# Performance work log

Measured on AMD Instinct MI355X. Metric: run time of the kernel, lower is better.

## Reference

```python
import jax, jax.numpy as jnp
import numpy as np

N_SRC = 50000
N_DST = 50000
N_EDGES = 1_600_000
D_IN = 128
D_OUT = 128
NUM_HEADS = 8
SCALE = float((D_OUT // NUM_HEADS) ** 0.5)


def setup_inputs() -> dict:
    key = jax.random.key(0)
    ks = jax.random.split(key, 10)
    s = 1.0 / np.sqrt(D_IN)
    return {
        "src_feat": jax.random.normal(ks[0], (N_SRC, D_IN), dtype=jnp.float32),
        "dst_feat": jax.random.normal(ks[1], (N_DST, D_OUT), dtype=jnp.float32),
        "src_idx": jax.random.randint(ks[2], (N_EDGES,), 0, N_SRC, dtype=jnp.int64),
        "dst_idx": jax.random.randint(ks[3], (N_EDGES,), 0, N_DST, dtype=jnp.int64),
        "Wq": jax.random.normal(ks[4], (D_OUT, D_OUT), dtype=jnp.float32) * s,
        "bq": jnp.zeros((D_OUT,), dtype=jnp.float32),
        "Wk": jax.random.normal(ks[5], (D_OUT, D_IN), dtype=jnp.float32) * s,
        "bk": jnp.zeros((D_OUT,), dtype=jnp.float32),
        "Wv": jax.random.normal(ks[6], (D_OUT, D_IN), dtype=jnp.float32) * s,
        "bv": jnp.zeros((D_OUT,), dtype=jnp.float32),
    }


def reference(src_feat, dst_feat, src_idx, dst_idx, Wq, bq, Wk, bk, Wv, bv):
    # Node-level projections (torch Linear: x @ W.T + b)
    Q = dst_feat @ Wq.T + bq            # [N_dst, D_OUT]
    K = src_feat @ Wk.T + bk            # [N_src, D_OUT]
    V = src_feat @ Wv.T + bv            # [N_src, D_OUT]

    # Edge-wise full-dim dot-product score (heads only affect the scale)
    score = jnp.sum(Q[dst_idx] * K[src_idx], axis=-1) / SCALE  # [E]

    # Segment softmax over incoming edges of each destination node
    m = jax.ops.segment_max(score, dst_idx, num_segments=N_DST)   # [N_dst]
    e = jnp.exp(score - m[dst_idx])                               # [E]
    denom = jax.ops.segment_sum(e, dst_idx, num_segments=N_DST)   # [N_dst]
    attn = e / denom[dst_idx]                                     # [E]

    # Weighted V scatter-sum to destination nodes
    out = jax.ops.segment_sum(attn[:, None] * V[src_idx], dst_idx,
                              num_segments=N_DST)                 # [N_dst, D_OUT]
    return out
```

## Files before the change

### kernel.cpp

```cpp
#include <hip/hip_runtime.h>
#include <hip/hip_bf16.h>


#define D 128
#define E1 4096
#define BCAP 10240
#define LOG2E 1.44269504088896340736f

typedef __attribute__((ext_vector_type(8))) short bf16x8;
typedef __attribute__((ext_vector_type(4))) float f32x4;
typedef __attribute__((ext_vector_type(4))) int v4i;
typedef __attribute__((ext_vector_type(4))) unsigned v4u;

static __device__ __forceinline__ unsigned short f2bf(float f) {
  unsigned u = __float_as_uint(f);
  u += 0x7fff + ((u >> 16) & 1);
  return (unsigned short)(u >> 16);
}
static __device__ __forceinline__ float bfl(unsigned u) {
  return __uint_as_float(u << 16);
}
static __device__ __forceinline__ float bfh(unsigned u) {
  return __uint_as_float(u & 0xffff0000u);
}

template <int CTRL>
static __device__ __forceinline__ float dpp_add(float x) {
  int y = __builtin_amdgcn_update_dpp(0, __float_as_int(x), CTRL, 0xF, 0xF, false);
  return x + __int_as_float(y);
}

static __device__ __forceinline__ float dot8(const float4& qa, const float4& qb,
                                             const v4u k0, const v4u k1) {
  return (qa.x * bfl(k0.x) + qa.y * bfh(k0.x) + qa.z * bfl(k0.y) +
          qa.w * bfh(k0.y)) +
         (qb.x * bfl(k1.x) + qb.y * bfh(k1.x) + qb.z * bfl(k1.y) +
          qb.w * bfh(k1.y));
}

static __device__ __forceinline__ void stage_w(const float* __restrict__ W,
                                               char* lds) {
  const int tid = threadIdx.x;
#pragma unroll
  for (int i = 0; i < 8; ++i) {
    const int g = i * 256 + tid;
    const int r = g >> 4, c16 = g & 15;
    const float4 w0 = *(const float4*)(W + r * 128 + c16 * 8);
    const float4 w1 = *(const float4*)(W + r * 128 + c16 * 8 + 4);
    bf16x8 b;
    b[0] = f2bf(w0.x); b[1] = f2bf(w0.y); b[2] = f2bf(w0.z); b[3] = f2bf(w0.w);
    b[4] = f2bf(w1.x); b[5] = f2bf(w1.y); b[6] = f2bf(w1.z); b[7] = f2bf(w1.w);
    *(bf16x8*)(lds + r * 256 + (((c16 ^ (r & 7)) << 4))) = b;
  }
}

static __device__ __forceinline__ bf16x8 ldw_lds(const char* lds, int n,
                                                 int colbyte) {
  return *(const bf16x8*)(lds + n * 256 + (colbyte ^ ((n & 7) << 4)));
}

static __device__ void bin1_body(
    int bx, int* h, int* basebuf, int* cur, const int* __restrict__ src_idx,
    const int* __restrict__ dst_idx, int* __restrict__ bins,
    int* __restrict__ bcount, int n) {
  const int tid = threadIdx.x;
  const int e0 = bx * E1;
  int dv[16], sv[16];
#pragma unroll
  for (int i = 0; i < 4; ++i) {
    int e = e0 + i * 1024 + tid * 4;
    if (e + 3 < n) {
      v4i d4 = __builtin_nontemporal_load((const v4i*)(dst_idx + e));
      v4i s4 = __builtin_nontemporal_load((const v4i*)(src_idx + e));
      dv[4 * i + 0] = d4.x; dv[4 * i + 1] = d4.y;
      dv[4 * i + 2] = d4.z; dv[4 * i + 3] = d4.w;
      sv[4 * i + 0] = s4.x; sv[4 * i + 1] = s4.y;
      sv[4 * i + 2] = s4.z; sv[4 * i + 3] = s4.w;
    } else {
      for (int k = 0; k < 4; ++k) {
        int ee = e + k;
        dv[4 * i + k] = (ee < n) ? dst_idx[ee] : -1;
        sv[4 * i + k] = (ee < n) ? src_idx[ee] : 0;
      }
    }
  }
  h[tid] = 0;
  __syncthreads();
#pragma unroll
  for (int i = 0; i < 16; ++i)
    if (dv[i] >= 0) atomicAdd(&h[dv[i] >> 8], 1);
  __syncthreads();
  const int c = h[tid];
  if (c > 0) basebuf[tid] = tid * BCAP + atomicAdd(&bcount[tid], c);
  cur[tid] = 0;
  __syncthreads();
#pragma unroll
  for (int i = 0; i < 16; ++i) {
    if (dv[i] >= 0) {
      const int b = dv[i] >> 8;
      const int r = atomicAdd(&cur[b], 1);
      const int off = basebuf[b] + r;
      if (off < (b + 1) * BCAP)
        bins[off] = sv[i] | ((dv[i] & 255) << 17);
    }
  }
}

static __device__ void bin2_body_1k(
    int b, int* smem, const int* __restrict__ bins,
    const int* __restrict__ bcount, int* __restrict__ csr,
    int* __restrict__ rowptr, int n_dst, int n_edges) {
  int* h = smem;
  int* ofs = smem + 256;
  int* cur = smem + 512;
  int* red = smem + 768;
  const int tid = threadIdx.x;

  if (tid < 256) red[tid] = (tid < b) ? min(bcount[tid], BCAP) : 0;
  __syncthreads();
  for (int off = 128; off > 0; off >>= 1) {
    if (tid < off) red[tid] += red[tid + off];
    __syncthreads();
  }
  const int gbase = red[0];
  const int cnt = min(bcount[b], BCAP);
  if (tid < 256) h[tid] = 0;
  __syncthreads();

  const int* bb = bins + b * BCAP;
  for (int i = tid; i < cnt; i += 1024) atomicAdd(&h[(bb[i] >> 17) & 255], 1);
  __syncthreads();

  const int myh = (tid < 256) ? h[tid] : 0;
  if (tid < 256) red[tid] = myh;
  __syncthreads();
  for (int off = 1; off < 256; off <<= 1) {
    int t = (tid >= off && tid < 256) ? red[tid - off] : 0;
    __syncthreads();
    if (tid < 256) red[tid] += t;
    __syncthreads();
  }
  if (tid < 256) {
    ofs[tid] = red[tid] - myh;
    cur[tid] = 0;
    const int d = b * 256 + tid;
    if (d < n_dst) rowptr[d] = gbase + ofs[tid];
    if (b == 0 && tid == 0) rowptr[n_dst] = n_edges;
  }
  __syncthreads();

  for (int i = tid; i < cnt; i += 1024) {
    const int p = bb[i];
    const int j = (p >> 17) & 255;
    const int r = atomicAdd(&cur[j], 1);
    csr[gbase + ofs[j] + r] = p & 0x1ffff;
  }
}

static __device__ void gemm_q_body(
    int bx, char* wlds, const float* __restrict__ X,
    const float* __restrict__ Wf, const float* __restrict__ bias,
    float* __restrict__ out, int N) {
  stage_w(Wf, wlds);
  __syncthreads();

  const int lane = threadIdx.x & 63;
  const int l15 = lane & 15, quad = lane >> 4;
  const int row0 = bx * 64 + (threadIdx.x >> 6) * 16;

  f32x4 acc[8];
#pragma unroll
  for (int t = 0; t < 8; ++t) acc[t] = (f32x4){0.f, 0.f, 0.f, 0.f};

  int ar = row0 + l15;
  if (ar >= N) ar = N - 1;
  const float* ap = X + (size_t)ar * D + quad * 8;

#pragma unroll
  for (int kc = 0; kc < 4; ++kc) {
    float4 a0 = *(const float4*)(ap + kc * 32);
    float4 a1 = *(const float4*)(ap + kc * 32 + 4);
    bf16x8 a;
    a[0] = f2bf(a0.x); a[1] = f2bf(a0.y); a[2] = f2bf(a0.z); a[3] = f2bf(a0.w);
    a[4] = f2bf(a1.x); a[5] = f2bf(a1.y); a[6] = f2bf(a1.z); a[7] = f2bf(a1.w);
    const int cb = kc * 64 + quad * 16;
#pragma unroll
    for (int t = 0; t < 8; ++t) {
      bf16x8 b = ldw_lds(wlds, t * 16 + l15, cb);
      acc[t] = __builtin_amdgcn_mfma_f32_16x16x32_bf16(a, b, acc[t], 0, 0, 0);
    }
  }
#pragma unroll
  for (int t = 0; t < 8; ++t) {
    const int c = t * 16 + l15;
    const float bc = bias[c];
#pragma unroll
    for (int r = 0; r < 4; ++r) {
      const int row = row0 + quad * 4 + r;
      if (row < N) out[(size_t)row * D + c] = acc[t][r] + bc;
    }
  }
}

static __device__ void gemm_kv_body(
    int bx, char* wlds, const float* __restrict__ X,
    const float* __restrict__ Wkf, const float* __restrict__ bk,
    const float* __restrict__ Wvf, const float* __restrict__ bv,
    unsigned short* __restrict__ KV, int N) {
  char* wk = wlds;
  char* wv = wlds + 32768;
  stage_w(Wkf, wk);
  stage_w(Wvf, wv);
  __syncthreads();

  const int tid = threadIdx.x;
  const int lane = tid & 63;
  const int l15 = lane & 15, quad = lane >> 4;
  const int wave = tid >> 6;
  const int row0 = bx * 64 + wave * 16;

  f32x4 accK[8], accV[8];
#pragma unroll
  for (int t = 0; t < 8; ++t) {
    accK[t] = (f32x4){0.f, 0.f, 0.f, 0.f};
    accV[t] = (f32x4){0.f, 0.f, 0.f, 0.f};
  }

  int ar = row0 + l15;
  if (ar >= N) ar = N - 1;
  const float* ap = X + (size_t)ar * D + quad * 8;

#pragma unroll
  for (int kc = 0; kc < 4; ++kc) {
    float4 a0 = *(const float4*)(ap + kc * 32);
    float4 a1 = *(const float4*)(ap + kc * 32 + 4);
    bf16x8 a;
    a[0] = f2bf(a0.x); a[1] = f2bf(a0.y); a[2] = f2bf(a0.z); a[3] = f2bf(a0.w);
    a[4] = f2bf(a1.x); a[5] = f2bf(a1.y); a[6] = f2bf(a1.z); a[7] = f2bf(a1.w);
    const int cb = kc * 64 + quad * 16;
#pragma unroll
    for (int t = 0; t < 8; ++t) {
      const int n = t * 16 + l15;
      bf16x8 b0 = ldw_lds(wk, n, cb);
      bf16x8 b1 = ldw_lds(wv, n, cb);
      accK[t] = __builtin_amdgcn_mfma_f32_16x16x32_bf16(a, b0, accK[t], 0, 0, 0);
      accV[t] = __builtin_amdgcn_mfma_f32_16x16x32_bf16(a, b1, accV[t], 0, 0, 0);
    }
  }

  __syncthreads();
  unsigned short (*stage)[256] = (unsigned short(*)[256])wlds;
#pragma unroll
  for (int t = 0; t < 8; ++t) {
    const int c = t * 16 + l15;
    const float bkc = bk[c], bvc = bv[c];
    const int ki = ((c >> 2) << 3) + (c & 3);
#pragma unroll
    for (int r = 0; r < 4; ++r) {
      const int lr = wave * 16 + quad * 4 + r;
      stage[lr][ki] = f2bf(accK[t][r] + bkc);
      stage[lr][ki + 4] = f2bf(accV[t][r] + bvc);
    }
  }
  __syncthreads();
  const int row_base = bx * 64;
#pragma unroll
  for (int i = 0; i < 8; ++i) {
    int idx = i * 256 + tid;
    int lr = idx >> 5;
    int c8 = (idx & 31) << 3;
    int grow = row_base + lr;
    if (grow < N)
      *(f32x4*)(KV + (size_t)grow * 256 + c8) = *(const f32x4*)&stage[lr][c8];
  }
}

static __device__ void fused_body(
    int v, const float* __restrict__ Q, const unsigned short* __restrict__ KV,
    const int* __restrict__ csr, const int* __restrict__ rowptr,
    float* __restrict__ out, int n_dst) {
  const int lane = threadIdx.x & 63;
  const int g = lane >> 4;
  const int gl = lane & 15;
  int d = v * 4 + (threadIdx.x >> 6);
  if (d >= n_dst) return;
  d = __builtin_amdgcn_readfirstlane(d);
  const int start = __builtin_amdgcn_readfirstlane(rowptr[d]);
  const int n = __builtin_amdgcn_readfirstlane(rowptr[d + 1]) - start;

  const float qs = 0.25f * LOG2E;
  float4 q0 = *(const float4*)(Q + (size_t)d * D + 4 * gl);
  float4 q1 = *(const float4*)(Q + (size_t)d * D + 64 + 4 * gl);
  q0.x *= qs; q0.y *= qs; q0.z *= qs; q0.w *= qs;
  q1.x *= qs; q1.y *= qs; q1.z *= qs; q1.w *= qs;

  f32x4 acc0 = (f32x4){0.f, 0.f, 0.f, 0.f};
  f32x4 acc1 = (f32x4){0.f, 0.f, 0.f, 0.f};
  float den = 0.f;
  const int* cp = csr + start;

  for (int base = 0; base < n; base += 64) {
    const int il = base + lane;
    const int iv = __builtin_nontemporal_load(cp + ((il < n) ? il : (n - 1)));
    const int m = min(64, n - base);
    for (int j = 0; j < m; j += 16) {
      const int s0 = __shfl(iv, j + g, 64);
      const int s1 = __shfl(iv, j + 4 + g, 64);
      const int s2 = __shfl(iv, j + 8 + g, 64);
      const int s3 = __shfl(iv, j + 12 + g, 64);
      const unsigned short* r0 = KV + (size_t)s0 * 256 + gl * 8;
      const unsigned short* r1 = KV + (size_t)s1 * 256 + gl * 8;
      const unsigned short* r2 = KV + (size_t)s2 * 256 + gl * 8;
      const unsigned short* r3 = KV + (size_t)s3 * 256 + gl * 8;
      const v4u a0 = *(const v4u*)(r0);
      const v4u a1 = *(const v4u*)(r0 + 128);
      const v4u b0 = *(const v4u*)(r1);
      const v4u b1 = *(const v4u*)(r1 + 128);
      const v4u c0 = *(const v4u*)(r2);
      const v4u c1 = *(const v4u*)(r2 + 128);
      const v4u e0 = *(const v4u*)(r3);
      const v4u e1 = *(const v4u*)(r3 + 128);

      float p0 = dot8(q0, q1, a0, a1);
      float p1 = dot8(q0, q1, b0, b1);
      float p2 = dot8(q0, q1, c0, c1);
      float p3 = dot8(q0, q1, e0, e1);

      p0 = dpp_add<0xB1>(p0);  p1 = dpp_add<0xB1>(p1);
      p2 = dpp_add<0xB1>(p2);  p3 = dpp_add<0xB1>(p3);
      p0 = dpp_add<0x4E>(p0);  p1 = dpp_add<0x4E>(p1);
      p2 = dpp_add<0x4E>(p2);  p3 = dpp_add<0x4E>(p3);
      p0 = dpp_add<0x141>(p0); p1 = dpp_add<0x141>(p1);
      p2 = dpp_add<0x141>(p2); p3 = dpp_add<0x141>(p3);
      p0 = dpp_add<0x140>(p0); p1 = dpp_add<0x140>(p1);
      p2 = dpp_add<0x140>(p2); p3 = dpp_add<0x140>(p3);

      const float w0 = (j + g < m)      ? exp2f(p0) : 0.f;
      const float w1 = (j + 4 + g < m)  ? exp2f(p1) : 0.f;
      const float w2 = (j + 8 + g < m)  ? exp2f(p2) : 0.f;
      const float w3 = (j + 12 + g < m) ? exp2f(p3) : 0.f;

      acc0[0] += w0 * bfl(a0.z) + w1 * bfl(b0.z) + w2 * bfl(c0.z) + w3 * bfl(e0.z);
      acc0[1] += w0 * bfh(a0.z) + w1 * bfh(b0.z) + w2 * bfh(c0.z) + w3 * bfh(e0.z);
      acc0[2] += w0 * bfl(a0.w) + w1 * bfl(b0.w) + w2 * bfl(c0.w) + w3 * bfl(e0.w);
      acc0[3] += w0 * bfh(a0.w) + w1 * bfh(b0.w) + w2 * bfh(c0.w) + w3 * bfh(e0.w);
      acc1[0] += w0 * bfl(a1.z) + w1 * bfl(b1.z) + w2 * bfl(c1.z) + w3 * bfl(e1.z);
      acc1[1] += w0 * bfh(a1.z) + w1 * bfh(b1.z) + w2 * bfh(c1.z) + w3 * bfh(e1.z);
      acc1[2] += w0 * bfl(a1.w) + w1 * bfl(b1.w) + w2 * bfl(c1.w) + w3 * bfl(e1.w);
      acc1[3] += w0 * bfh(a1.w) + w1 * bfh(b1.w) + w2 * bfh(c1.w) + w3 * bfh(e1.w);
      den += (w0 + w1) + (w2 + w3);
    }
  }

#pragma unroll
  for (int msk = 16; msk <= 32; msk <<= 1) {
    acc0[0] += __shfl_xor(acc0[0], msk, 64);
    acc0[1] += __shfl_xor(acc0[1], msk, 64);
    acc0[2] += __shfl_xor(acc0[2], msk, 64);
    acc0[3] += __shfl_xor(acc0[3], msk, 64);
    acc1[0] += __shfl_xor(acc1[0], msk, 64);
    acc1[1] += __shfl_xor(acc1[1], msk, 64);
    acc1[2] += __shfl_xor(acc1[2], msk, 64);
    acc1[3] += __shfl_xor(acc1[3], msk, 64);
    den += __shfl_xor(den, msk, 64);
  }

  if (lane < 16) {
    const float r = (n > 0) ? 1.0f / den : 0.f;
    f32x4 o0 = (f32x4){acc0[0] * r, acc0[1] * r, acc0[2] * r, acc0[3] * r};
    f32x4 o1 = (f32x4){acc1[0] * r, acc1[1] * r, acc1[2] * r, acc1[3] * r};
    __builtin_nontemporal_store(o0, (f32x4*)(out + (size_t)d * D + 4 * gl));
    __builtin_nontemporal_store(o1,
                                (f32x4*)(out + (size_t)d * D + 64 + 4 * gl));
  }
}


__global__ __launch_bounds__(256) void front_kernel(
    const int* __restrict__ src_idx, const int* __restrict__ dst_idx,
    int* __restrict__ bins, int* __restrict__ bcount, int n_edges,
    const float* __restrict__ dst_feat, const float* __restrict__ Wq,
    const float* __restrict__ bq, float* __restrict__ Q, int n_dst,
    const float* __restrict__ src_feat, const float* __restrict__ Wk,
    const float* __restrict__ bk, const float* __restrict__ Wv,
    const float* __restrict__ bv, unsigned short* __restrict__ KV, int n_src,
    int g1, int gq) {
  __shared__ char wlds[65536];
  const int b = blockIdx.x;
  if (b < g1) {
    int* sh = (int*)wlds;
    bin1_body(b, sh, sh + 256, sh + 512, src_idx, dst_idx, bins, bcount,
              n_edges);
  } else if (b < g1 + gq) {
    gemm_q_body(b - g1, wlds, dst_feat, Wq, bq, Q, n_dst);
  } else {
    gemm_kv_body(b - g1 - gq, wlds, src_feat, Wk, bk, Wv, bv, KV, n_src);
  }
}

__global__ __launch_bounds__(1024) void bin2_kernel(
    const int* __restrict__ bins, const int* __restrict__ bcount,
    int* __restrict__ csr, int* __restrict__ rowptr, int n_dst, int n_edges) {
  __shared__ int sh[1024];
  bin2_body_1k(blockIdx.x, sh, bins, bcount, csr, rowptr, n_dst, n_edges);
}

__global__ __launch_bounds__(256) void fused_agg_kernel(
    const float* __restrict__ Q, const unsigned short* __restrict__ KV,
    const int* __restrict__ csr, const int* __restrict__ rowptr,
    float* __restrict__ out, int n_dst) {
  fused_body(blockIdx.x, Q, KV, csr, rowptr, out, n_dst);
}

extern "C" void kernel_launch(void* const* d_in, const int* in_sizes, int n_in,
                              void* d_out, int out_size, void* d_ws,
                              size_t ws_size, hipStream_t stream) {
  const float* src_feat = (const float*)d_in[0];
  const float* dst_feat = (const float*)d_in[1];
  const int* src_idx = (const int*)d_in[2];
  const int* dst_idx = (const int*)d_in[3];
  const float* Wq = (const float*)d_in[4];
  const float* bq = (const float*)d_in[5];
  const float* Wk = (const float*)d_in[6];
  const float* bk = (const float*)d_in[7];
  const float* Wv = (const float*)d_in[8];
  const float* bv = (const float*)d_in[9];

  const int n_src = in_sizes[0] / D;
  const int n_dst = in_sizes[1] / D;
  const int n_edges = in_sizes[2];
  const int nbk = (n_dst + 255) >> 8;

  float* out = (float*)d_out;

  float* Q = (float*)d_ws;
  unsigned short* KV = (unsigned short*)(Q + (size_t)n_dst * D);
  int* bcount = (int*)(KV + (size_t)n_src * 256);
  int* rowptr = bcount + 256;
  int* csr = rowptr + (n_dst + 1);
  int* bins = csr + n_edges;

  (void)hipMemsetAsync(bcount, 0, 256 * sizeof(int), stream);

  dim3 blk(256);
  const int g1 = (n_edges + E1 - 1) / E1;
  const int gq = (n_dst + 63) / 64;
  const int gkv = (n_src + 63) / 64;
  const int nf = (n_dst + 3) / 4;

  front_kernel<<<dim3(g1 + gq + gkv), blk, 0, stream>>>(
      src_idx, dst_idx, bins, bcount, n_edges, dst_feat, Wq, bq, Q, n_dst,
      src_feat, Wk, bk, Wv, bv, KV, n_src, g1, gq);

  bin2_kernel<<<dim3(nbk), dim3(1024), 0, stream>>>(bins, bcount, csr, rowptr,
                                                    n_dst, n_edges);

  fused_agg_kernel<<<dim3(nf), blk, 0, stream>>>(Q, KV, csr, rowptr, out,
                                                 n_dst);
}
```

Before: 267.0 us.

## Split bin2 buckets into quarters and amortize weight staging over 256-row GEMM blocks

The second binning pass now launches four 512-thread blocks per bucket. Each block rebuilds the bucket histogram but writes only the CSR entries and rowptr values for its own quarter of destinations, which spreads the work over more CUs. The Q and KV projection blocks each process 256 rows in four 64-row chunks, so the weight matrices are staged into LDS once per 256 rows instead of once per 64. KV output staging moves to a separate LDS region and is written out in half-tiles, raising front-kernel LDS to 80KB, which may reduce occupancy for the binning blocks that share that kernel.

```diff
diff --git a/kernel.cpp b/kernel.cpp
--- a/kernel.cpp
+++ b/kernel.cpp
@@ -106,29 +106,31 @@
   }
 }
 
-static __device__ void bin2_body_1k(
+static __device__ void bin2_body_q(
     int b, int* smem, const int* __restrict__ bins,
     const int* __restrict__ bcount, int* __restrict__ csr,
     int* __restrict__ rowptr, int n_dst, int n_edges) {
+  const int bucket = b >> 2;
+  const int quarter = b & 3;
   int* h = smem;
   int* ofs = smem + 256;
   int* cur = smem + 512;
   int* red = smem + 768;
   const int tid = threadIdx.x;
 
-  if (tid < 256) red[tid] = (tid < b) ? min(bcount[tid], BCAP) : 0;
+  if (tid < 256) red[tid] = (tid < bucket) ? min(bcount[tid], BCAP) : 0;
   __syncthreads();
   for (int off = 128; off > 0; off >>= 1) {
     if (tid < off) red[tid] += red[tid + off];
     __syncthreads();
   }
   const int gbase = red[0];
-  const int cnt = min(bcount[b], BCAP);
+  const int cnt = min(bcount[bucket], BCAP);
   if (tid < 256) h[tid] = 0;
   __syncthreads();
 
-  const int* bb = bins + b * BCAP;
-  for (int i = tid; i < cnt; i += 1024) atomicAdd(&h[(bb[i] >> 17) & 255], 1);
+  const int* bb = bins + bucket * BCAP;
+  for (int i = tid; i < cnt; i += 512) atomicAdd(&h[(bb[i] >> 17) & 255], 1);
   __syncthreads();
 
   const int myh = (tid < 256) ? h[tid] : 0;
@@ -143,17 +145,19 @@
   if (tid < 256) {
     ofs[tid] = red[tid] - myh;
     cur[tid] = 0;
-    const int d = b * 256 + tid;
-    if (d < n_dst) rowptr[d] = gbase + ofs[tid];
-    if (b == 0 && tid == 0) rowptr[n_dst] = n_edges;
-  }
-  __syncthreads();
-
-  for (int i = tid; i < cnt; i += 1024) {
+    const int d = bucket * 256 + tid;
+    if ((tid >> 6) == quarter && d < n_dst) rowptr[d] = gbase + ofs[tid];
+  }
+  if (b == 0 && tid == 0) rowptr[n_dst] = n_edges;
+  __syncthreads();
+
+  for (int i = tid; i < cnt; i += 512) {
     const int p = bb[i];
     const int j = (p >> 17) & 255;
-    const int r = atomicAdd(&cur[j], 1);
-    csr[gbase + ofs[j] + r] = p & 0x1ffff;
+    if ((j >> 6) == quarter) {
+      const int r = atomicAdd(&cur[j], 1);
+      csr[gbase + ofs[j] + r] = p & 0x1ffff;
+    }
   }
 }
 
@@ -166,38 +170,42 @@
 
   const int lane = threadIdx.x & 63;
   const int l15 = lane & 15, quad = lane >> 4;
-  const int row0 = bx * 64 + (threadIdx.x >> 6) * 16;
-
-  f32x4 acc[8];
-#pragma unroll
-  for (int t = 0; t < 8; ++t) acc[t] = (f32x4){0.f, 0.f, 0.f, 0.f};
-
-  int ar = row0 + l15;
-  if (ar >= N) ar = N - 1;
-  const float* ap = X + (size_t)ar * D + quad * 8;
-
-#pragma unroll
-  for (int kc = 0; kc < 4; ++kc) {
-    float4 a0 = *(const float4*)(ap + kc * 32);
-    float4 a1 = *(const float4*)(ap + kc * 32 + 4);
-    bf16x8 a;
-    a[0] = f2bf(a0.x); a[1] = f2bf(a0.y); a[2] = f2bf(a0.z); a[3] = f2bf(a0.w);
-    a[4] = f2bf(a1.x); a[5] = f2bf(a1.y); a[6] = f2bf(a1.z); a[7] = f2bf(a1.w);
-    const int cb = kc * 64 + quad * 16;
+  const int wave = threadIdx.x >> 6;
+
+#pragma unroll
+  for (int ch = 0; ch < 4; ++ch) {
+    const int row0 = bx * 256 + ch * 64 + wave * 16;
+    f32x4 acc[8];
+#pragma unroll
+    for (int t = 0; t < 8; ++t) acc[t] = (f32x4){0.f, 0.f, 0.f, 0.f};
+
+    int ar = row0 + l15;
+    if (ar >= N) ar = N - 1;
+    const float* ap = X + (size_t)ar * D + quad * 8;
+
+#pragma unroll
+    for (int kc = 0; kc < 4; ++kc) {
+      float4 a0 = *(const float4*)(ap + kc * 32);
+      float4 a1 = *(const float4*)(ap + kc * 32 + 4);
+      bf16x8 a;
+      a[0] = f2bf(a0.x); a[1] = f2bf(a0.y); a[2] = f2bf(a0.z); a[3] = f2bf(a0.w);
+      a[4] = f2bf(a1.x); a[5] = f2bf(a1.y); a[6] = f2bf(a1.z); a[7] = f2bf(a1.w);
+      const int cb = kc * 64 + quad * 16;
+#pragma unroll
+      for (int t = 0; t < 8; ++t) {
+        bf16x8 b = ldw_lds(wlds, t * 16 + l15, cb);
+        acc[t] = __builtin_amdgcn_mfma_f32_16x16x32_bf16(a, b, acc[t], 0, 0, 0);
+      }
+    }
 #pragma unroll
     for (int t = 0; t < 8; ++t) {
-      bf16x8 b = ldw_lds(wlds, t * 16 + l15, cb);
-      acc[t] = __builtin_amdgcn_mfma_f32_16x16x32_bf16(a, b, acc[t], 0, 0, 0);
-    }
-  }
-#pragma unroll
-  for (int t = 0; t < 8; ++t) {
-    const int c = t * 16 + l15;
-    const float bc = bias[c];
-#pragma unroll
-    for (int r = 0; r < 4; ++r) {
-      const int row = row0 + quad * 4 + r;
-      if (row < N) out[(size_t)row * D + c] = acc[t][r] + bc;
+      const int c = t * 16 + l15;
+      const float bc = bias[c];
+#pragma unroll
+      for (int r = 0; r < 4; ++r) {
+        const int row = row0 + quad * 4 + r;
+        if (row < N) out[(size_t)row * D + c] = acc[t][r] + bc;
+      }
     }
   }
 }
@@ -209,6 +217,7 @@
     unsigned short* __restrict__ KV, int N) {
   char* wk = wlds;
   char* wv = wlds + 32768;
+  unsigned short (*stage)[256] = (unsigned short(*)[256])(wlds + 65536);
   stage_w(Wkf, wk);
   stage_w(Wvf, wv);
   __syncthreads();
@@ -217,61 +226,71 @@
   const int lane = tid & 63;
   const int l15 = lane & 15, quad = lane >> 4;
   const int wave = tid >> 6;
-  const int row0 = bx * 64 + wave * 16;
-
-  f32x4 accK[8], accV[8];
-#pragma unroll
-  for (int t = 0; t < 8; ++t) {
-    accK[t] = (f32x4){0.f, 0.f, 0.f, 0.f};
-    accV[t] = (f32x4){0.f, 0.f, 0.f, 0.f};
-  }
-
-  int ar = row0 + l15;
-  if (ar >= N) ar = N - 1;
-  const float* ap = X + (size_t)ar * D + quad * 8;
-
-#pragma unroll
-  for (int kc = 0; kc < 4; ++kc) {
-    float4 a0 = *(const float4*)(ap + kc * 32);
-    float4 a1 = *(const float4*)(ap + kc * 32 + 4);
-    bf16x8 a;
-    a[0] = f2bf(a0.x); a[1] = f2bf(a0.y); a[2] = f2bf(a0.z); a[3] = f2bf(a0.w);
-    a[4] = f2bf(a1.x); a[5] = f2bf(a1.y); a[6] = f2bf(a1.z); a[7] = f2bf(a1.w);
-    const int cb = kc * 64 + quad * 16;
+
+#pragma unroll
+  for (int ch = 0; ch < 4; ++ch) {
+    const int row0 = bx * 256 + ch * 64 + wave * 16;
+    f32x4 accK[8], accV[8];
 #pragma unroll
     for (int t = 0; t < 8; ++t) {
-      const int n = t * 16 + l15;
-      bf16x8 b0 = ldw_lds(wk, n, cb);
-      bf16x8 b1 = ldw_lds(wv, n, cb);
-      accK[t] = __builtin_amdgcn_mfma_f32_16x16x32_bf16(a, b0, accK[t], 0, 0, 0);
-      accV[t] = __builtin_amdgcn_mfma_f32_16x16x32_bf16(a, b1, accV[t], 0, 0, 0);
-    }
-  }
-
-  __syncthreads();
-  unsigned short (*stage)[256] = (unsigned short(*)[256])wlds;
-#pragma unroll
-  for (int t = 0; t < 8; ++t) {
-    const int c = t * 16 + l15;
-    const float bkc = bk[c], bvc = bv[c];
-    const int ki = ((c >> 2) << 3) + (c & 3);
-#pragma unroll
-    for (int r = 0; r < 4; ++r) {
-      const int lr = wave * 16 + quad * 4 + r;
-      stage[lr][ki] = f2bf(accK[t][r] + bkc);
-      stage[lr][ki + 4] = f2bf(accV[t][r] + bvc);
-    }
-  }
-  __syncthreads();
-  const int row_base = bx * 64;
-#pragma unroll
-  for (int i = 0; i < 8; ++i) {
-    int idx = i * 256 + tid;
-    int lr = idx >> 5;
-    int c8 = (idx & 31) << 3;
-    int grow = row_base + lr;
-    if (grow < N)
-      *(f32x4*)(KV + (size_t)grow * 256 + c8) = *(const f32x4*)&stage[lr][c8];
+      accK[t] = (f32x4){0.f, 0.f, 0.f, 0.f};
+      accV[t] = (f32x4){0.f, 0.f, 0.f, 0.f};
+    }
+
+    int ar = row0 + l15;
+    if (ar >= N) ar = N - 1;
+    const float* ap = X + (size_t)ar * D + quad * 8;
+
+#pragma unroll
+    for (int kc = 0; kc < 4; ++kc) {
+      float4 a0 = *(const float4*)(ap + kc * 32);
+      float4 a1 = *(const float4*)(ap + kc * 32 + 4);
+      bf16x8 a;
+      a[0] = f2bf(a0.x); a[1] = f2bf(a0.y); a[2] = f2bf(a0.z); a[3] = f2bf(a0.w);
+      a[4] = f2bf(a1.x); a[5] = f2bf(a1.y); a[6] = f2bf(a1.z); a[7] = f2bf(a1.w);
+      const int cb = kc * 64 + quad * 16;
+#pragma unroll
+      for (int t = 0; t < 8; ++t) {
+        const int n = t * 16 + l15;
+        bf16x8 b0 = ldw_lds(wk, n, cb);
+        bf16x8 b1 = ldw_lds(wv, n, cb);
+        accK[t] =
+            __builtin_amdgcn_mfma_f32_16x16x32_bf16(a, b0, accK[t], 0, 0, 0);
+        accV[t] =
+            __builtin_amdgcn_mfma_f32_16x16x32_bf16(a, b1, accV[t], 0, 0, 0);
+      }
+    }
+
+    const int row_base = bx * 256 + ch * 64;
+#pragma unroll
+    for (int half = 0; half < 2; ++half) {
+      if ((wave >> 1) == half) {
+#pragma unroll
+        for (int t = 0; t < 8; ++t) {
+          const int c = t * 16 + l15;
+          const float bkc = bk[c], bvc = bv[c];
+          const int ki = ((c >> 2) << 3) + (c & 3);
+#pragma unroll
+          for (int r = 0; r < 4; ++r) {
+            const int lr = (wave & 1) * 16 + quad * 4 + r;
+            stage[lr][ki] = f2bf(accK[t][r] + bkc);
+            stage[lr][ki + 4] = f2bf(accV[t][r] + bvc);
+          }
+        }
+      }
+      __syncthreads();
+#pragma unroll
+      for (int i = 0; i < 4; ++i) {
+        int idx = i * 256 + tid;
+        int lr = idx >> 5;
+        int c8 = (idx & 31) << 3;
+        int grow = row_base + half * 32 + lr;
+        if (grow < N)
+          *(f32x4*)(KV + (size_t)grow * 256 + c8) =
+              *(const f32x4*)&stage[lr][c8];
+      }
+      __syncthreads();
+    }
   }
 }
 
@@ -384,25 +403,25 @@
     const float* __restrict__ src_feat, const float* __restrict__ Wk,
     const float* __restrict__ bk, const float* __restrict__ Wv,
     const float* __restrict__ bv, unsigned short* __restrict__ KV, int n_src,
-    int g1, int gq) {
-  __shared__ char wlds[65536];
+    int g1, int gq4) {
+  __shared__ char wlds[81920];
   const int b = blockIdx.x;
   if (b < g1) {
     int* sh = (int*)wlds;
     bin1_body(b, sh, sh + 256, sh + 512, src_idx, dst_idx, bins, bcount,
               n_edges);
-  } else if (b < g1 + gq) {
+  } else if (b < g1 + gq4) {
     gemm_q_body(b - g1, wlds, dst_feat, Wq, bq, Q, n_dst);
   } else {
-    gemm_kv_body(b - g1 - gq, wlds, src_feat, Wk, bk, Wv, bv, KV, n_src);
-  }
-}
-
-__global__ __launch_bounds__(1024) void bin2_kernel(
+    gemm_kv_body(b - g1 - gq4, wlds, src_feat, Wk, bk, Wv, bv, KV, n_src);
+  }
+}
+
+__global__ __launch_bounds__(512) void bin2_kernel(
     const int* __restrict__ bins, const int* __restrict__ bcount,
     int* __restrict__ csr, int* __restrict__ rowptr, int n_dst, int n_edges) {
   __shared__ int sh[1024];
-  bin2_body_1k(blockIdx.x, sh, bins, bcount, csr, rowptr, n_dst, n_edges);
+  bin2_body_q(blockIdx.x, sh, bins, bcount, csr, rowptr, n_dst, n_edges);
 }
 
 __global__ __launch_bounds__(256) void fused_agg_kernel(
@@ -444,16 +463,16 @@
 
   dim3 blk(256);
   const int g1 = (n_edges + E1 - 1) / E1;
-  const int gq = (n_dst + 63) / 64;
-  const int gkv = (n_src + 63) / 64;
+  const int gq4 = (n_dst + 255) / 256;
+  const int gkv4 = (n_src + 255) / 256;
   const int nf = (n_dst + 3) / 4;
 
-  front_kernel<<<dim3(g1 + gq + gkv), blk, 0, stream>>>(
+  front_kernel<<<dim3(g1 + gq4 + gkv4), blk, 0, stream>>>(
       src_idx, dst_idx, bins, bcount, n_edges, dst_feat, Wq, bq, Q, n_dst,
-      src_feat, Wk, bk, Wv, bv, KV, n_src, g1, gq);
-
-  bin2_kernel<<<dim3(nbk), dim3(1024), 0, stream>>>(bins, bcount, csr, rowptr,
-                                                    n_dst, n_edges);
+      src_feat, Wk, bk, Wv, bv, KV, n_src, g1, gq4);
+
+  bin2_kernel<<<dim3(4 * nbk), dim3(512), 0, stream>>>(bins, bcount, csr,
+                                                       rowptr, n_dst, n_edges);
 
   fused_agg_kernel<<<dim3(nf), blk, 0, stream>>>(Q, KV, csr, rowptr, out,
                                                  n_dst);
```

Measured after the change: 278.6 us. +4.4%, slower.

## Halve KV GEMM LDS footprint by staging weights in two output-column halves

Applied to the files above, without the earlier changes.

The K/V projection GEMM now stages Wk and Wv into LDS in two 64-row halves instead of all at once, so the front kernel's shared array drops from 64KB to 32KB. The A fragments are loaded and converted to bf16 up front and held in registers across both halves. The smaller LDS allocation is meant to let more blocks share a CU across the fused binning, Q-GEMM and KV-GEMM blocks. In exchange it adds an extra pair of barriers and staging passes per block, and raises register pressure from keeping four A fragments live.

```diff
diff --git a/kernel.cpp b/kernel.cpp
--- a/kernel.cpp
+++ b/kernel.cpp
@@ -47,6 +47,23 @@
     const int r = g >> 4, c16 = g & 15;
     const float4 w0 = *(const float4*)(W + r * 128 + c16 * 8);
     const float4 w1 = *(const float4*)(W + r * 128 + c16 * 8 + 4);
+    bf16x8 b;
+    b[0] = f2bf(w0.x); b[1] = f2bf(w0.y); b[2] = f2bf(w0.z); b[3] = f2bf(w0.w);
+    b[4] = f2bf(w1.x); b[5] = f2bf(w1.y); b[6] = f2bf(w1.z); b[7] = f2bf(w1.w);
+    *(bf16x8*)(lds + r * 256 + (((c16 ^ (r & 7)) << 4))) = b;
+  }
+}
+
+static __device__ __forceinline__ void stage_w_half(const float* __restrict__ W,
+                                                    char* lds, int h) {
+  const int tid = threadIdx.x;
+#pragma unroll
+  for (int i = 0; i < 4; ++i) {
+    const int g = i * 256 + tid;
+    const int r = g >> 4, c16 = g & 15;
+    const float* wp = W + (size_t)(h * 64 + r) * 128 + c16 * 8;
+    const float4 w0 = *(const float4*)(wp);
+    const float4 w1 = *(const float4*)(wp + 4);
     bf16x8 b;
     b[0] = f2bf(w0.x); b[1] = f2bf(w0.y); b[2] = f2bf(w0.z); b[3] = f2bf(w0.w);
     b[4] = f2bf(w1.x); b[5] = f2bf(w1.y); b[6] = f2bf(w1.z); b[7] = f2bf(w1.w);
@@ -208,17 +225,27 @@
     const float* __restrict__ Wvf, const float* __restrict__ bv,
     unsigned short* __restrict__ KV, int N) {
   char* wk = wlds;
-  char* wv = wlds + 32768;
-  stage_w(Wkf, wk);
-  stage_w(Wvf, wv);
-  __syncthreads();
-
+  char* wv = wlds + 16384;
   const int tid = threadIdx.x;
   const int lane = tid & 63;
   const int l15 = lane & 15, quad = lane >> 4;
   const int wave = tid >> 6;
   const int row0 = bx * 64 + wave * 16;
 
+  int ar = row0 + l15;
+  if (ar >= N) ar = N - 1;
+  const float* ap = X + (size_t)ar * D + quad * 8;
+  bf16x8 afrag[4];
+#pragma unroll
+  for (int kc = 0; kc < 4; ++kc) {
+    float4 a0 = *(const float4*)(ap + kc * 32);
+    float4 a1 = *(const float4*)(ap + kc * 32 + 4);
+    afrag[kc][0] = f2bf(a0.x); afrag[kc][1] = f2bf(a0.y);
+    afrag[kc][2] = f2bf(a0.z); afrag[kc][3] = f2bf(a0.w);
+    afrag[kc][4] = f2bf(a1.x); afrag[kc][5] = f2bf(a1.y);
+    afrag[kc][6] = f2bf(a1.z); afrag[kc][7] = f2bf(a1.w);
+  }
+
   f32x4 accK[8], accV[8];
 #pragma unroll
   for (int t = 0; t < 8; ++t) {
@@ -226,25 +253,27 @@
     accV[t] = (f32x4){0.f, 0.f, 0.f, 0.f};
   }
 
-  int ar = row0 + l15;
-  if (ar >= N) ar = N - 1;
-  const float* ap = X + (size_t)ar * D + quad * 8;
-
-#pragma unroll
-  for (int kc = 0; kc < 4; ++kc) {
-    float4 a0 = *(const float4*)(ap + kc * 32);
-    float4 a1 = *(const float4*)(ap + kc * 32 + 4);
-    bf16x8 a;
-    a[0] = f2bf(a0.x); a[1] = f2bf(a0.y); a[2] = f2bf(a0.z); a[3] = f2bf(a0.w);
-    a[4] = f2bf(a1.x); a[5] = f2bf(a1.y); a[6] = f2bf(a1.z); a[7] = f2bf(a1.w);
-    const int cb = kc * 64 + quad * 16;
-#pragma unroll
-    for (int t = 0; t < 8; ++t) {
-      const int n = t * 16 + l15;
-      bf16x8 b0 = ldw_lds(wk, n, cb);
-      bf16x8 b1 = ldw_lds(wv, n, cb);
-      accK[t] = __builtin_amdgcn_mfma_f32_16x16x32_bf16(a, b0, accK[t], 0, 0, 0);
-      accV[t] = __builtin_amdgcn_mfma_f32_16x16x32_bf16(a, b1, accV[t], 0, 0, 0);
+#pragma unroll
+  for (int h = 0; h < 2; ++h) {
+    __syncthreads();
+    stage_w_half(Wkf, wk, h);
+    stage_w_half(Wvf, wv, h);
+    __syncthreads();
+#pragma unroll
+    for (int kc = 0; kc < 4; ++kc) {
+      const int cb = kc * 64 + quad * 16;
+#pragma unroll
+      for (int t = 0; t < 4; ++t) {
+        const int n = t * 16 + l15;
+        bf16x8 b0 = ldw_lds(wk, n, cb);
+        bf16x8 b1 = ldw_lds(wv, n, cb);
+        accK[h * 4 + t] =
+            __builtin_amdgcn_mfma_f32_16x16x32_bf16(afrag[kc], b0,
+                                                    accK[h * 4 + t], 0, 0, 0);
+        accV[h * 4 + t] =
+            __builtin_amdgcn_mfma_f32_16x16x32_bf16(afrag[kc], b1,
+                                                    accV[h * 4 + t], 0, 0, 0);
+      }
     }
   }
 
@@ -385,7 +414,7 @@
     const float* __restrict__ bk, const float* __restrict__ Wv,
     const float* __restrict__ bv, unsigned short* __restrict__ KV, int n_src,
     int g1, int gq) {
-  __shared__ char wlds[65536];
+  __shared__ char wlds[32768];
   const int b = blockIdx.x;
   if (b < g1) {
     int* sh = (int*)wlds;
```

Result: no change. 265.2 us (-0.7%).

## Rebalance front kernels: move KV GEMM alongside bin2, use 1024-thread blocks

Applied to the files above, without the earlier changes.

Splits the former front kernel so the first launch does only edge binning plus the Q projection, while the K/V projection runs in the same launch as the second binning pass (bin2). All front blocks become 1024 threads, with each GEMM block covering 256 rows and staging the weights once per block. Activation loads are issued before weight staging so global reads overlap the LDS fill. The aim is to cut weight restaging and to balance work across the two launches. The cost is larger blocks with higher register pressure, and the KV output staging now takes two passes.

```diff
diff --git a/kernel.cpp b/kernel.cpp
--- a/kernel.cpp
+++ b/kernel.cpp
@@ -38,12 +38,17 @@
           qb.w * bfh(k1.y));
 }
 
-static __device__ __forceinline__ void stage_w(const float* __restrict__ W,
-                                               char* lds) {
+static __device__ __forceinline__ bf16x8 ldw_lds(const char* lds, int n,
+                                                 int colbyte) {
+  return *(const bf16x8*)(lds + n * 256 + (colbyte ^ ((n & 7) << 4)));
+}
+
+static __device__ __forceinline__ void stage_w_1k(const float* __restrict__ W,
+                                                  char* lds) {
   const int tid = threadIdx.x;
 #pragma unroll
-  for (int i = 0; i < 8; ++i) {
-    const int g = i * 256 + tid;
+  for (int i = 0; i < 2; ++i) {
+    const int g = i * 1024 + tid;
     const int r = g >> 4, c16 = g & 15;
     const float4 w0 = *(const float4*)(W + r * 128 + c16 * 8);
     const float4 w1 = *(const float4*)(W + r * 128 + c16 * 8 + 4);
@@ -54,48 +59,39 @@
   }
 }
 
-static __device__ __forceinline__ bf16x8 ldw_lds(const char* lds, int n,
-                                                 int colbyte) {
-  return *(const bf16x8*)(lds + n * 256 + (colbyte ^ ((n & 7) << 4)));
-}
-
-static __device__ void bin1_body(
+static __device__ void bin1_body_1k(
     int bx, int* h, int* basebuf, int* cur, const int* __restrict__ src_idx,
     const int* __restrict__ dst_idx, int* __restrict__ bins,
     int* __restrict__ bcount, int n) {
   const int tid = threadIdx.x;
-  const int e0 = bx * E1;
-  int dv[16], sv[16];
+  const int e = bx * E1 + tid * 4;
+  int dv[4], sv[4];
+  if (e + 3 < n) {
+    v4i d4 = __builtin_nontemporal_load((const v4i*)(dst_idx + e));
+    v4i s4 = __builtin_nontemporal_load((const v4i*)(src_idx + e));
+    dv[0] = d4.x; dv[1] = d4.y; dv[2] = d4.z; dv[3] = d4.w;
+    sv[0] = s4.x; sv[1] = s4.y; sv[2] = s4.z; sv[3] = s4.w;
+  } else {
+    for (int k = 0; k < 4; ++k) {
+      int ee = e + k;
+      dv[k] = (ee < n) ? dst_idx[ee] : -1;
+      sv[k] = (ee < n) ? src_idx[ee] : 0;
+    }
+  }
+  if (tid < 256) h[tid] = 0;
+  __syncthreads();
+#pragma unroll
+  for (int i = 0; i < 4; ++i)
+    if (dv[i] >= 0) atomicAdd(&h[dv[i] >> 8], 1);
+  __syncthreads();
+  if (tid < 256) {
+    const int c = h[tid];
+    if (c > 0) basebuf[tid] = tid * BCAP + atomicAdd(&bcount[tid], c);
+    cur[tid] = 0;
+  }
+  __syncthreads();
 #pragma unroll
   for (int i = 0; i < 4; ++i) {
-    int e = e0 + i * 1024 + tid * 4;
-    if (e + 3 < n) {
-      v4i d4 = __builtin_nontemporal_load((const v4i*)(dst_idx + e));
-      v4i s4 = __builtin_nontemporal_load((const v4i*)(src_idx + e));
-      dv[4 * i + 0] = d4.x; dv[4 * i + 1] = d4.y;
-      dv[4 * i + 2] = d4.z; dv[4 * i + 3] = d4.w;
-      sv[4 * i + 0] = s4.x; sv[4 * i + 1] = s4.y;
-      sv[4 * i + 2] = s4.z; sv[4 * i + 3] = s4.w;
-    } else {
-      for (int k = 0; k < 4; ++k) {
-        int ee = e + k;
-        dv[4 * i + k] = (ee < n) ? dst_idx[ee] : -1;
-        sv[4 * i + k] = (ee < n) ? src_idx[ee] : 0;
-      }
-    }
-  }
-  h[tid] = 0;
-  __syncthreads();
-#pragma unroll
-  for (int i = 0; i < 16; ++i)
-    if (dv[i] >= 0) atomicAdd(&h[dv[i] >> 8], 1);
-  __syncthreads();
-  const int c = h[tid];
-  if (c > 0) basebuf[tid] = tid * BCAP + atomicAdd(&bcount[tid], c);
-  cur[tid] = 0;
-  __syncthreads();
-#pragma unroll
-  for (int i = 0; i < 16; ++i) {
     if (dv[i] >= 0) {
       const int b = dv[i] >> 8;
       const int r = atomicAdd(&cur[b], 1);
@@ -157,32 +153,40 @@
   }
 }
 
-static __device__ void gemm_q_body(
+static __device__ void gemm_q_1k(
     int bx, char* wlds, const float* __restrict__ X,
     const float* __restrict__ Wf, const float* __restrict__ bias,
     float* __restrict__ out, int N) {
-  stage_w(Wf, wlds);
-  __syncthreads();
-
-  const int lane = threadIdx.x & 63;
+  const int tid = threadIdx.x;
+  const int lane = tid & 63;
   const int l15 = lane & 15, quad = lane >> 4;
-  const int row0 = bx * 64 + (threadIdx.x >> 6) * 16;
-
-  f32x4 acc[8];
-#pragma unroll
-  for (int t = 0; t < 8; ++t) acc[t] = (f32x4){0.f, 0.f, 0.f, 0.f};
+  const int wave = tid >> 6;
+  const int row0 = bx * 256 + wave * 16;
 
   int ar = row0 + l15;
   if (ar >= N) ar = N - 1;
   const float* ap = X + (size_t)ar * D + quad * 8;
-
+  float4 p0[4], p1[4];
 #pragma unroll
   for (int kc = 0; kc < 4; ++kc) {
-    float4 a0 = *(const float4*)(ap + kc * 32);
-    float4 a1 = *(const float4*)(ap + kc * 32 + 4);
+    p0[kc] = *(const float4*)(ap + kc * 32);
+    p1[kc] = *(const float4*)(ap + kc * 32 + 4);
+  }
+
+  stage_w_1k(Wf, wlds);
+  __syncthreads();
+
+  f32x4 acc[8];
+#pragma unroll
+  for (int t = 0; t < 8; ++t) acc[t] = (f32x4){0.f, 0.f, 0.f, 0.f};
+
+#pragma unroll
+  for (int kc = 0; kc < 4; ++kc) {
     bf16x8 a;
-    a[0] = f2bf(a0.x); a[1] = f2bf(a0.y); a[2] = f2bf(a0.z); a[3] = f2bf(a0.w);
-    a[4] = f2bf(a1.x); a[5] = f2bf(a1.y); a[6] = f2bf(a1.z); a[7] = f2bf(a1.w);
+    a[0] = f2bf(p0[kc].x); a[1] = f2bf(p0[kc].y);
+    a[2] = f2bf(p0[kc].z); a[3] = f2bf(p0[kc].w);
+    a[4] = f2bf(p1[kc].x); a[5] = f2bf(p1[kc].y);
+    a[6] = f2bf(p1[kc].z); a[7] = f2bf(p1[kc].w);
     const int cb = kc * 64 + quad * 16;
 #pragma unroll
     for (int t = 0; t < 8; ++t) {
@@ -202,22 +206,36 @@
   }
 }
 
-static __device__ void gemm_kv_body(
+static __device__ void gemm_kv_1k(
     int bx, char* wlds, const float* __restrict__ X,
     const float* __restrict__ Wkf, const float* __restrict__ bk,
     const float* __restrict__ Wvf, const float* __restrict__ bv,
     unsigned short* __restrict__ KV, int N) {
   char* wk = wlds;
   char* wv = wlds + 32768;
-  stage_w(Wkf, wk);
-  stage_w(Wvf, wv);
-  __syncthreads();
-
   const int tid = threadIdx.x;
   const int lane = tid & 63;
   const int l15 = lane & 15, quad = lane >> 4;
   const int wave = tid >> 6;
-  const int row0 = bx * 64 + wave * 16;
+  const int row0 = bx * 256 + wave * 16;
+
+  int ar = row0 + l15;
+  if (ar >= N) ar = N - 1;
+  const float* ap = X + (size_t)ar * D + quad * 8;
+  bf16x8 afrag[4];
+#pragma unroll
+  for (int kc = 0; kc < 4; ++kc) {
+    float4 a0 = *(const float4*)(ap + kc * 32);
+    float4 a1 = *(const float4*)(ap + kc * 32 + 4);
+    afrag[kc][0] = f2bf(a0.x); afrag[kc][1] = f2bf(a0.y);
+    afrag[kc][2] = f2bf(a0.z); afrag[kc][3] = f2bf(a0.w);
+    afrag[kc][4] = f2bf(a1.x); afrag[kc][5] = f2bf(a1.y);
+    afrag[kc][6] = f2bf(a1.z); afrag[kc][7] = f2bf(a1.w);
+  }
+
+  stage_w_1k(Wkf, wk);
+  stage_w_1k(Wvf, wv);
+  __syncthreads();
 
   f32x4 accK[8], accV[8];
 #pragma unroll
@@ -226,52 +244,50 @@
     accV[t] = (f32x4){0.f, 0.f, 0.f, 0.f};
   }
 
-  int ar = row0 + l15;
-  if (ar >= N) ar = N - 1;
-  const float* ap = X + (size_t)ar * D + quad * 8;
-
 #pragma unroll
   for (int kc = 0; kc < 4; ++kc) {
-    float4 a0 = *(const float4*)(ap + kc * 32);
-    float4 a1 = *(const float4*)(ap + kc * 32 + 4);
-    bf16x8 a;
-    a[0] = f2bf(a0.x); a[1] = f2bf(a0.y); a[2] = f2bf(a0.z); a[3] = f2bf(a0.w);
-    a[4] = f2bf(a1.x); a[5] = f2bf(a1.y); a[6] = f2bf(a1.z); a[7] = f2bf(a1.w);
     const int cb = kc * 64 + quad * 16;
 #pragma unroll
     for (int t = 0; t < 8; ++t) {
       const int n = t * 16 + l15;
       bf16x8 b0 = ldw_lds(wk, n, cb);
       bf16x8 b1 = ldw_lds(wv, n, cb);
-      accK[t] = __builtin_amdgcn_mfma_f32_16x16x32_bf16(a, b0, accK[t], 0, 0, 0);
-      accV[t] = __builtin_amdgcn_mfma_f32_16x16x32_bf16(a, b1, accV[t], 0, 0, 0);
-    }
-  }
-
-  __syncthreads();
+      accK[t] =
+          __builtin_amdgcn_mfma_f32_16x16x32_bf16(afrag[kc], b0, accK[t], 0, 0, 0);
+      accV[t] =
+          __builtin_amdgcn_mfma_f32_16x16x32_bf16(afrag[kc], b1, accV[t], 0, 0, 0);
+    }
+  }
+
   unsigned short (*stage)[256] = (unsigned short(*)[256])wlds;
 #pragma unroll
-  for (int t = 0; t < 8; ++t) {
-    const int c = t * 16 + l15;
-    const float bkc = bk[c], bvc = bv[c];
-    const int ki = ((c >> 2) << 3) + (c & 3);
-#pragma unroll
-    for (int r = 0; r < 4; ++r) {
-      const int lr = wave * 16 + quad * 4 + r;
-      stage[lr][ki] = f2bf(accK[t][r] + bkc);
-      stage[lr][ki + 4] = f2bf(accV[t][r] + bvc);
-    }
-  }
-  __syncthreads();
-  const int row_base = bx * 64;
-#pragma unroll
-  for (int i = 0; i < 8; ++i) {
-    int idx = i * 256 + tid;
-    int lr = idx >> 5;
-    int c8 = (idx & 31) << 3;
-    int grow = row_base + lr;
-    if (grow < N)
-      *(f32x4*)(KV + (size_t)grow * 256 + c8) = *(const f32x4*)&stage[lr][c8];
+  for (int p = 0; p < 2; ++p) {
+    __syncthreads();
+    if ((wave >> 3) == p) {
+#pragma unroll
+      for (int t = 0; t < 8; ++t) {
+        const int c = t * 16 + l15;
+        const float bkc = bk[c], bvc = bv[c];
+        const int ki = ((c >> 2) << 3) + (c & 3);
+#pragma unroll
+        for (int r = 0; r < 4; ++r) {
+          const int lr = (wave & 7) * 16 + quad * 4 + r;
+          stage[lr][ki] = f2bf(accK[t][r] + bkc);
+          stage[lr][ki + 4] = f2bf(accV[t][r] + bvc);
+        }
+      }
+    }
+    __syncthreads();
+    const int row_base = bx * 256 + p * 128;
+#pragma unroll
+    for (int i = 0; i < 4; ++i) {
+      int idx = i * 1024 + tid;
+      int lr = idx >> 5;
+      int c8 = (idx & 31) << 3;
+      int grow = row_base + lr;
+      if (grow < N)
+        *(f32x4*)(KV + (size_t)grow * 256 + c8) = *(const f32x4*)&stage[lr][c8];
+    }
   }
 }
 
@@ -376,33 +392,36 @@
 }
 
 
-__global__ __launch_bounds__(256) void front_kernel(
+__global__ __launch_bounds__(1024) void d1_kernel(
     const int* __restrict__ src_idx, const int* __restrict__ dst_idx,
     int* __restrict__ bins, int* __restrict__ bcount, int n_edges,
     const float* __restrict__ dst_feat, const float* __restrict__ Wq,
-    const float* __restrict__ bq, float* __restrict__ Q, int n_dst,
+    const float* __restrict__ bq, float* __restrict__ Q, int n_dst, int g1) {
+  __shared__ char wlds[32768];
+  const int b = blockIdx.x;
+  if (b < g1) {
+    int* sh = (int*)wlds;
+    bin1_body_1k(b, sh, sh + 256, sh + 512, src_idx, dst_idx, bins, bcount,
+                 n_edges);
+  } else {
+    gemm_q_1k(b - g1, wlds, dst_feat, Wq, bq, Q, n_dst);
+  }
+}
+
+__global__ __launch_bounds__(1024) void d2_kernel(
+    const int* __restrict__ bins, const int* __restrict__ bcount,
+    int* __restrict__ csr, int* __restrict__ rowptr, int n_dst, int n_edges,
     const float* __restrict__ src_feat, const float* __restrict__ Wk,
     const float* __restrict__ bk, const float* __restrict__ Wv,
     const float* __restrict__ bv, unsigned short* __restrict__ KV, int n_src,
-    int g1, int gq) {
+    int nbk) {
   __shared__ char wlds[65536];
   const int b = blockIdx.x;
-  if (b < g1) {
-    int* sh = (int*)wlds;
-    bin1_body(b, sh, sh + 256, sh + 512, src_idx, dst_idx, bins, bcount,
-              n_edges);
-  } else if (b < g1 + gq) {
-    gemm_q_body(b - g1, wlds, dst_feat, Wq, bq, Q, n_dst);
+  if (b < nbk) {
+    bin2_body_1k(b, (int*)wlds, bins, bcount, csr, rowptr, n_dst, n_edges);
   } else {
-    gemm_kv_body(b - g1 - gq, wlds, src_feat, Wk, bk, Wv, bv, KV, n_src);
-  }
-}
-
-__global__ __launch_bounds__(1024) void bin2_kernel(
-    const int* __restrict__ bins, const int* __restrict__ bcount,
-    int* __restrict__ csr, int* __restrict__ rowptr, int n_dst, int n_edges) {
-  __shared__ int sh[1024];
-  bin2_body_1k(blockIdx.x, sh, bins, bcount, csr, rowptr, n_dst, n_edges);
+    gemm_kv_1k(b - nbk, wlds, src_feat, Wk, bk, Wv, bv, KV, n_src);
+  }
 }
 
 __global__ __launch_bounds__(256) void fused_agg_kernel(
@@ -442,19 +461,18 @@
 
   (void)hipMemsetAsync(bcount, 0, 256 * sizeof(int), stream);
 
-  dim3 blk(256);
   const int g1 = (n_edges + E1 - 1) / E1;
-  const int gq = (n_dst + 63) / 64;
-  const int gkv = (n_src + 63) / 64;
+  const int gq1k = (n_dst + 255) / 256;
+  const int gkv1k = (n_src + 255) / 256;
   const int nf = (n_dst + 3) / 4;
 
-  front_kernel<<<dim3(g1 + gq + gkv), blk, 0, stream>>>(
-      src_idx, dst_idx, bins, bcount, n_edges, dst_feat, Wq, bq, Q, n_dst,
-      src_feat, Wk, bk, Wv, bv, KV, n_src, g1, gq);
-
-  bin2_kernel<<<dim3(nbk), dim3(1024), 0, stream>>>(bins, bcount, csr, rowptr,
-                                                    n_dst, n_edges);
-
-  fused_agg_kernel<<<dim3(nf), blk, 0, stream>>>(Q, KV, csr, rowptr, out,
-                                                 n_dst);
-}
+  d1_kernel<<<dim3(g1 + gq1k), dim3(1024), 0, stream>>>(
+      src_idx, dst_idx, bins, bcount, n_edges, dst_feat, Wq, bq, Q, n_dst, g1);
+
+  d2_kernel<<<dim3(nbk + gkv1k), dim3(1024), 0, stream>>>(
+      bins, bcount, csr, rowptr, n_dst, n_edges, src_feat, Wk, bk, Wv, bv, KV,
+      n_src, nbk);
+
+  fused_agg_kernel<<<dim3(nf), dim3(256), 0, stream>>>(Q, KV, csr, rowptr, out,
+                                                       n_dst);
+}
```

Result: no change. 263.3 us (-1.4%).
